# Optimization experiments

Hardware: AMD Instinct MI355X
Metric: run time of the kernel (lower is better)

## Reference

```python
import jax, jax.numpy as jnp
import numpy as np

EPS = 1e-5
NEG_INF = float('-inf')

B, L, D = 4, 1024, 1024
H = 16
HD = D // H
I = 3280  # _round_to_multiple(3.2 * 1024, 8)
WIN = 256
STD = 0.01


def rmsnorm(x, w):
    x = jnp.clip(x.astype(jnp.float32), -10000.0, 10000.0)
    rms = jnp.sqrt(jnp.maximum(jnp.mean(x * x, axis=-1, keepdims=True), EPS) + EPS)
    out = x / rms * w
    return jnp.where(jnp.isfinite(out), out, jnp.zeros_like(out))


def setup_inputs() -> dict:
    key = jax.random.key(0)
    ks = jax.random.split(key, 12)
    inp = {
        'x': jax.random.normal(ks[0], (B, L, D), dtype=jnp.float32),
        'wq_w': jax.random.normal(ks[1], (D, D), dtype=jnp.float32) * STD,
        'wq_b': jnp.zeros((D,), jnp.float32),
        'wk_w': jax.random.normal(ks[2], (D, D), dtype=jnp.float32) * STD,
        'wk_b': jnp.zeros((D,), jnp.float32),
        'wv_w': jax.random.normal(ks[3], (D, D), dtype=jnp.float32) * STD,
        'wv_b': jnp.zeros((D,), jnp.float32),
        'wo_w': jax.random.normal(ks[4], (D, D), dtype=jnp.float32) * STD,
        'wo_b': jnp.zeros((D,), jnp.float32),
        'q_norm_w': jnp.ones((HD,), jnp.float32),
        'k_norm_w': jnp.ones((HD,), jnp.float32),
        'seq_norm_w': jnp.ones((D,), jnp.float32),
        'seq_post_norm_w': jnp.ones((D,), jnp.float32),
        'ffn_norm_w': jnp.ones((D,), jnp.float32),
        'ffn_post_norm_w': jnp.ones((D,), jnp.float32),
        'w1_w': jax.random.normal(ks[5], (I, D), dtype=jnp.float32) * STD,
        'w1_b': jnp.zeros((I,), jnp.float32),
        'w2_w': jax.random.normal(ks[6], (D, I), dtype=jnp.float32) * STD,
        'w2_b': jnp.zeros((D,), jnp.float32),
        'w3_w': jax.random.normal(ks[7], (I, D), dtype=jnp.float32) * STD,
        'w3_b': jnp.zeros((I,), jnp.float32),
        'window_size': WIN,
    }
    return inp


def attention(x, wq_w, wq_b, wk_w, wk_b, wv_w, wv_b, wo_w, wo_b, q_norm_w, k_norm_w, window_size):
    b, l, d = x.shape
    x = x.astype(jnp.float32)
    q = (x @ wq_w.T + wq_b).reshape(b, l, H, HD)
    k = (x @ wk_w.T + wk_b).reshape(b, l, H, HD)
    v = (x @ wv_w.T + wv_b).reshape(b, l, H, HD)
    q = rmsnorm(q, q_norm_w)
    k = rmsnorm(k, k_norm_w)
    scale = HD ** -0.5
    scores = jnp.einsum('blhd,bmhd->bhlm', q, k) * scale
    i = jnp.arange(l)[:, None]
    j = jnp.arange(l)[None, :]
    masked = (j > i) | (i - j >= window_size)  # True => forbidden
    scores = scores + jnp.where(masked, NEG_INF, 0.0)
    p = jax.nn.softmax(scores, axis=-1)
    attn = jnp.einsum('bhlm,bmhd->blhd', p, v)
    attn = jnp.where(jnp.isfinite(attn), attn, jnp.zeros_like(attn))
    attn = attn.reshape(b, l, d)
    return attn @ wo_w.T + wo_b


def swiglu(x, w1_w, w1_b, w2_w, w2_b, w3_w, w3_b):
    x = x.astype(jnp.float32)
    z1 = x @ w1_w.T + w1_b
    z3 = x @ w3_w.T + w3_b
    return (jax.nn.silu(z1) * z3) @ w2_w.T + w2_b


def reference(x, wq_w, wq_b, wk_w, wk_b, wv_w, wv_b, wo_w, wo_b,
              q_norm_w, k_norm_w, seq_norm_w, seq_post_norm_w,
              ffn_norm_w, ffn_post_norm_w,
              w1_w, w1_b, w2_w, w2_b, w3_w, w3_b, window_size):
    # seq_norm -> attn -> seq_post_norm -> residual
    a = attention(rmsnorm(x, seq_norm_w), wq_w, wq_b, wk_w, wk_b, wv_w, wv_b,
                  wo_w, wo_b, q_norm_w, k_norm_w, window_size)
    h = x + rmsnorm(a, seq_post_norm_w)
    # ffn_norm -> ffn -> ffn_post_norm -> residual
    f = swiglu(rmsnorm(h, ffn_norm_w), w1_w, w1_b, w2_w, w2_b, w3_w, w3_b)
    return h + rmsnorm(f, ffn_post_norm_w)
```

## Files before the change

kernel.cpp:

```cpp
#include <hip/hip_runtime.h>
#include <cmath>
#include <cstdint>

typedef __bf16 bf16;
typedef bf16 bf16x4 __attribute__((ext_vector_type(4)));
typedef bf16 bf16x8 __attribute__((ext_vector_type(8)));
typedef float f32x4 __attribute__((ext_vector_type(4)));
typedef unsigned int u32;
typedef u32 u32x4 __attribute__((ext_vector_type(4)));

#define EPS 1e-5f

__device__ __forceinline__ float clipf(float v) {
    return fminf(fmaxf(v, -10000.0f), 10000.0f);
}
__device__ __forceinline__ float fin0(float v) { return isfinite(v) ? v : 0.0f; }

__device__ __forceinline__ void async_copy16(void* lds, const void* g) {
    __builtin_amdgcn_global_load_lds((__attribute__((address_space(1))) void*)(void*)g,
                                     (__attribute__((address_space(3))) void*)lds,
                                     16, 0, 0);
}

__global__ __launch_bounds__(256) void prep(const float* __restrict__ wq, const float* __restrict__ wk,
                                            const float* __restrict__ wv, const float* __restrict__ wo,
                                            bf16* __restrict__ Wq, bf16* __restrict__ Wk,
                                            bf16* __restrict__ Wv, bf16* __restrict__ Wo,
                                            const float* __restrict__ w1, const float* __restrict__ w3,
                                            bf16* __restrict__ Wf,
                                            const float* __restrict__ w2, bf16* __restrict__ W2p,
                                            const float* __restrict__ x, const float* __restrict__ snw,
                                            bf16* __restrict__ xn) {
    const int bid = blockIdx.x, t = threadIdx.x;
    if (bid < 4096) {
        int z = bid >> 10, r = bid & 1023;
        const float* in = (z == 0) ? wq : (z == 1) ? wk : (z == 2) ? wv : wo;
        bf16* out = (z == 0) ? Wq : (z == 1) ? Wk : (z == 2) ? Wv : Wo;
        f32x4 v = ((const f32x4*)(in + (size_t)r * 1024))[t];
        bf16x4 o = {(bf16)v[0], (bf16)v[1], (bf16)v[2], (bf16)v[3]};
        ((bf16x4*)(out + (size_t)r * 1024))[t] = o;
    } else if (bid < 10752) {
        int ri = bid - 4096;
        int lc = ((ri >> 5) << 4) + (ri & 15);
        const float* in = ((ri >> 4) & 1) ? w3 : w1;
        bf16x4 o = {(bf16)0.f, (bf16)0.f, (bf16)0.f, (bf16)0.f};
        if (lc < 3280) {
            f32x4 v = ((const f32x4*)(in + (size_t)lc * 1024))[t];
            o[0] = (bf16)v[0]; o[1] = (bf16)v[1]; o[2] = (bf16)v[2]; o[3] = (bf16)v[3];
        }
        ((bf16x4*)(Wf + (size_t)ri * 1024))[t] = o;
    } else if (bid < 11776) {
        int r = bid - 10752;
        for (int c4 = t * 4; c4 < 3328; c4 += 1024) {
            bf16x4 o = {(bf16)0.f, (bf16)0.f, (bf16)0.f, (bf16)0.f};
            if (c4 + 3 < 3280) {
                f32x4 v = *(const f32x4*)(w2 + (size_t)r * 3280 + c4);
                o[0] = (bf16)v[0]; o[1] = (bf16)v[1]; o[2] = (bf16)v[2]; o[3] = (bf16)v[3];
            } else {
                #pragma unroll
                for (int j = 0; j < 4; ++j)
                    if (c4 + j < 3280) o[j] = (bf16)w2[(size_t)r * 3280 + c4 + j];
            }
            *(bf16x4*)(W2p + (size_t)r * 3328 + c4) = o;
        }
    } else {
        __shared__ float sred[4];
        int row = bid - 11776;
        f32x4 xv = ((const f32x4*)(x + (size_t)row * 1024))[t];
        f32x4 cv;
        cv[0] = clipf(xv[0]); cv[1] = clipf(xv[1]); cv[2] = clipf(xv[2]); cv[3] = clipf(xv[3]);
        float ss = cv[0]*cv[0] + cv[1]*cv[1] + cv[2]*cv[2] + cv[3]*cv[3];
        #pragma unroll
        for (int off = 32; off >= 1; off >>= 1) ss += __shfl_xor(ss, off, 64);
        if ((t & 63) == 0) sred[t >> 6] = ss;
        __syncthreads();
        float tot = sred[0] + sred[1] + sred[2] + sred[3];
        float rms = sqrtf(fmaxf(tot * (1.0f / 1024.0f), EPS) + EPS);
        f32x4 wv_ = ((const f32x4*)snw)[t];
        bf16x4 o;
        o[0] = (bf16)fin0(cv[0] / rms * wv_[0]);
        o[1] = (bf16)fin0(cv[1] / rms * wv_[1]);
        o[2] = (bf16)fin0(cv[2] / rms * wv_[2]);
        o[3] = (bf16)fin0(cv[3] / rms * wv_[3]);
        *(bf16x4*)(xn + (size_t)row * 1024 + t * 4) = o;
    }
}

__global__ __launch_bounds__(256) void gemm_qkv(const bf16* __restrict__ A,
                                                const bf16* __restrict__ B0,
                                                const bf16* __restrict__ B1,
                                                const bf16* __restrict__ B2,
                                                const float* __restrict__ g0,
                                                const float* __restrict__ g1,
                                                const float* __restrict__ g2,
                                                const float* __restrict__ qnw,
                                                const float* __restrict__ knw,
                                                bf16* __restrict__ C0,
                                                bf16* __restrict__ C1,
                                                bf16* __restrict__ VT) {
    const int z = blockIdx.z;
    const bf16* B = (z == 0) ? B0 : (z == 1) ? B1 : B2;
    const float* bias = (z == 0) ? g0 : (z == 1) ? g1 : g2;
    const float* hw = (z == 0) ? qnw : knw;

    __shared__ __align__(16) bf16 sA[2][128 * 32];
    __shared__ __align__(16) bf16 sB[2][128 * 32];
    const int tid = threadIdx.x;
    const int w = tid >> 6, lane = tid & 63;
    const int m0 = blockIdx.x * 128;
    const int n0 = blockIdx.y * 128;
    const int mwo = (w >> 1) * 64, nwo = (w & 1) * 64;
    const int r16 = lane & 15, quad = lane >> 4;
    const int kreg = quad * 8;
    const int K = 1024, N = 1024;

    f32x4 zero = {0.f, 0.f, 0.f, 0.f};
    f32x4 acc[4][4];
    #pragma unroll
    for (int i = 0; i < 4; ++i)
        #pragma unroll
        for (int j = 0; j < 4; ++j) acc[i][j] = zero;

    const int c0 = tid, c1 = tid + 256;
    const int am0 = c0 >> 2, ak0 = (c0 & 3) << 3;
    const int am1 = c1 >> 2, ak1 = (c1 & 3) << 3;

    {
        async_copy16(&sA[0][c0 * 8], &A[(size_t)(m0 + am0) * K + ak0]);
        async_copy16(&sA[0][c1 * 8], &A[(size_t)(m0 + am1) * K + ak1]);
        async_copy16(&sB[0][c0 * 8], &B[(size_t)(n0 + am0) * K + ak0]);
        async_copy16(&sB[0][c1 * 8], &B[(size_t)(n0 + am1) * K + ak1]);
    }
    for (int kt = 0; kt < 32; ++kt) {
        __syncthreads();
        const int cur = kt & 1, nxt = cur ^ 1;
        if (kt + 1 < 32) {
            const int kb = (kt + 1) << 5;
            async_copy16(&sA[nxt][c0 * 8], &A[(size_t)(m0 + am0) * K + kb + ak0]);
            async_copy16(&sA[nxt][c1 * 8], &A[(size_t)(m0 + am1) * K + kb + ak1]);
            async_copy16(&sB[nxt][c0 * 8], &B[(size_t)(n0 + am0) * K + kb + ak0]);
            async_copy16(&sB[nxt][c1 * 8], &B[(size_t)(n0 + am1) * K + kb + ak1]);
        }
        bf16x8 af[4], bfr[4];
        #pragma unroll
        for (int i = 0; i < 4; ++i) {
            af[i]  = *(const bf16x8*)&sA[cur][(mwo + i * 16 + r16) * 32 + kreg];
            bfr[i] = *(const bf16x8*)&sB[cur][(nwo + i * 16 + r16) * 32 + kreg];
        }
        #pragma unroll
        for (int mi = 0; mi < 4; ++mi)
            #pragma unroll
            for (int ni = 0; ni < 4; ++ni)
                acc[mi][ni] = __builtin_amdgcn_mfma_f32_16x16x32_bf16(af[mi], bfr[ni], acc[mi][ni], 0, 0, 0);
    }

    float bv[4];
    #pragma unroll
    for (int ni = 0; ni < 4; ++ni) bv[ni] = bias[n0 + nwo + ni * 16 + r16];

    if (z < 2) {
        bf16* C = (z == 0) ? C0 : C1;
        float nwv[4];
        #pragma unroll
        for (int ni = 0; ni < 4; ++ni) nwv[ni] = hw[ni * 16 + r16];
        #pragma unroll
        for (int mi = 0; mi < 4; ++mi) {
            #pragma unroll
            for (int r = 0; r < 4; ++r) {
                float v[4], ss = 0.0f;
                #pragma unroll
                for (int ni = 0; ni < 4; ++ni) {
                    v[ni] = clipf(acc[mi][ni][r] + bv[ni]);
                    ss += v[ni] * v[ni];
                }
                ss += __shfl_xor(ss, 1, 64);
                ss += __shfl_xor(ss, 2, 64);
                ss += __shfl_xor(ss, 4, 64);
                ss += __shfl_xor(ss, 8, 64);
                float rms = sqrtf(fmaxf(ss * (1.0f / 64.0f), EPS) + EPS);
                int row = m0 + mwo + mi * 16 + quad * 4 + r;
                #pragma unroll
                for (int ni = 0; ni < 4; ++ni) {
                    int col = n0 + nwo + ni * 16 + r16;
                    C[(size_t)row * N + col] = (bf16)fin0(v[ni] / rms * nwv[ni]);
                }
            }
        }
    } else {
        const int b_ = m0 >> 10;
        const int tokbase = (m0 & 1023) + mwo;
        #pragma unroll
        for (int ni = 0; ni < 4; ++ni) {
            int col = n0 + nwo + ni * 16 + r16;
            int h_ = col >> 6, hd = col & 63;
            bf16* dst = VT + (((size_t)b_ * 16 + h_) * 64 + hd) * 1024;
            #pragma unroll
            for (int mi = 0; mi < 4; ++mi) {
                bf16x4 pack;
                #pragma unroll
                for (int r = 0; r < 4; ++r) pack[r] = (bf16)(acc[mi][ni][r] + bv[ni]);
                *(bf16x4*)&dst[tokbase + mi * 16 + quad * 4] = pack;
            }
        }
    }
}

__global__ __launch_bounds__(256) void attn_win(const bf16* __restrict__ q,
                                                const bf16* __restrict__ k,
                                                const bf16* __restrict__ vt,
                                                const int* __restrict__ winp,
                                                bf16* __restrict__ o) {
    __shared__ __align__(16) bf16 sQ[64 * 64];
    __shared__ __align__(16) bf16 sK[64 * 64];
    __shared__ __align__(16) bf16 sVt[64 * 80];
    __shared__ __align__(16) bf16 sP[64 * 64];
    const int tid = threadIdx.x, w = tid >> 6, lane = tid & 63;
    const int qt = blockIdx.x, h = blockIdx.y, b = blockIdx.z;
    const int q0 = qt * 64;
    const int win = *winp;
    const float scale = 0.125f;
    const int r16 = lane & 15, quad = lane >> 4;

    {
        int qr0 = tid >> 3, col0 = (tid & 7) * 8;
        async_copy16(&sQ[tid * 8], &q[(((size_t)b * 1024 + q0 + qr0) * 16 + h) * 64 + col0]);
        int c1 = tid + 256;
        int qr1 = c1 >> 3, col1 = (c1 & 7) * 8;
        async_copy16(&sQ[c1 * 8], &q[(((size_t)b * 1024 + q0 + qr1) * 16 + h) * 64 + col1]);
    }
    __syncthreads();
    bf16x8 aq0 = *(const bf16x8*)&sQ[(w * 16 + r16) * 64 + quad * 8];
    bf16x8 aq1 = *(const bf16x8*)&sQ[(w * 16 + r16) * 64 + 32 + quad * 8];

    float Lr[4];
    f32x4 zero = {0.f, 0.f, 0.f, 0.f};
    f32x4 accO[4];
    #pragma unroll
    for (int r = 0; r < 4; ++r) Lr[r] = 0.0f;
    #pragma unroll
    for (int nf = 0; nf < 4; ++nf) accO[nf] = zero;

    int lo = q0 - (win - 1); if (lo < 0) lo = 0;
    const int kt0 = lo >> 6;
    const bf16* vth = vt + ((size_t)b * 16 + h) * 64 * 1024;

    for (int kt = kt0; kt <= qt; ++kt) {
        __syncthreads();
        {
            int col0 = (tid & 7) * 8;
            async_copy16(&sK[tid * 8], &k[(((size_t)b * 1024 + kt * 64 + (tid >> 3)) * 16 + h) * 64 + col0]);
            int c1 = tid + 256;
            int col1 = (c1 & 7) * 8;
            async_copy16(&sK[c1 * 8], &k[(((size_t)b * 1024 + kt * 64 + (c1 >> 3)) * 16 + h) * 64 + col1]);
        }
        #pragma unroll
        for (int c = tid; c < 512; c += 256) {
            int hd = c >> 3, koff = (c & 7) * 8;
            *(u32x4*)&sVt[hd * 80 + koff] = *(const u32x4*)&vth[(size_t)hd * 1024 + kt * 64 + koff];
        }
        __syncthreads();

        f32x4 sf[4];
        #pragma unroll
        for (int nf = 0; nf < 4; ++nf) {
            bf16x8 bk0 = *(const bf16x8*)&sK[(nf * 16 + r16) * 64 + quad * 8];
            bf16x8 bk1 = *(const bf16x8*)&sK[(nf * 16 + r16) * 64 + 32 + quad * 8];
            f32x4 accS = zero;
            accS = __builtin_amdgcn_mfma_f32_16x16x32_bf16(aq0, bk0, accS, 0, 0, 0);
            accS = __builtin_amdgcn_mfma_f32_16x16x32_bf16(aq1, bk1, accS, 0, 0, 0);
            sf[nf] = accS;
        }

        #pragma unroll
        for (int r = 0; r < 4; ++r) {
            int i = q0 + w * 16 + quad * 4 + r;
            float ps = 0.0f;
            #pragma unroll
            for (int nf = 0; nf < 4; ++nf) {
                int j = kt * 64 + nf * 16 + r16;
                bool ok = (j <= i) && (i - j < win);
                float pv = ok ? __expf(sf[nf][r] * scale - 8.0f) : 0.0f;
                ps += pv;
                sP[(w * 16 + quad * 4 + r) * 64 + nf * 16 + r16] = (bf16)pv;
            }
            Lr[r] += ps;
        }
        __syncthreads();

        bf16x8 ap0 = *(const bf16x8*)&sP[(w * 16 + r16) * 64 + quad * 8];
        bf16x8 ap1 = *(const bf16x8*)&sP[(w * 16 + r16) * 64 + 32 + quad * 8];
        #pragma unroll
        for (int nf = 0; nf < 4; ++nf) {
            bf16x8 bv0 = *(const bf16x8*)&sVt[(nf * 16 + r16) * 80 + quad * 8];
            bf16x8 bv1 = *(const bf16x8*)&sVt[(nf * 16 + r16) * 80 + 32 + quad * 8];
            accO[nf] = __builtin_amdgcn_mfma_f32_16x16x32_bf16(ap0, bv0, accO[nf], 0, 0, 0);
            accO[nf] = __builtin_amdgcn_mfma_f32_16x16x32_bf16(ap1, bv1, accO[nf], 0, 0, 0);
        }
    }

    #pragma unroll
    for (int r = 0; r < 4; ++r) {
        float l = Lr[r];
        l += __shfl_xor(l, 1, 64);
        l += __shfl_xor(l, 2, 64);
        l += __shfl_xor(l, 4, 64);
        l += __shfl_xor(l, 8, 64);
        float inv = (l > 0.0f) ? 1.0f / l : 0.0f;
        int row = q0 + w * 16 + quad * 4 + r;
        #pragma unroll
        for (int nf = 0; nf < 4; ++nf) {
            float ov = fin0(accO[nf][r] * inv);
            o[(((size_t)b * 1024 + row) * 16 + h) * 64 + nf * 16 + r16] = (bf16)ov;
        }
    }
}

__global__ __launch_bounds__(512) void gemm_sk2(const bf16* __restrict__ A,
                                                const bf16* __restrict__ B,
                                                float* __restrict__ P,
                                                int K, int Kh) {
    __shared__ __align__(16) bf16 sA[2][256 * 32];
    __shared__ __align__(16) bf16 sB[2][128 * 32];
    const int tid = threadIdx.x;
    const int w = tid >> 6, lane = tid & 63;
    const int m0 = blockIdx.x * 256, n0 = blockIdx.y * 128;
    const int mwo = (w & 3) * 64, nwo = (w >> 2) * 64;
    const int r16 = lane & 15, quad = lane >> 4, kreg = quad * 8;
    const int kbase = blockIdx.z * Kh;
    const int N = 1024;

    const int ar0 = tid >> 2,        ak0 = (tid & 3) << 3;
    const int c1 = tid + 512;
    const int ar1 = c1 >> 2,         ak1 = (c1 & 3) << 3;
    const int br = tid >> 2,         bk = (tid & 3) << 3;

    f32x4 zero = {0.f, 0.f, 0.f, 0.f};
    f32x4 acc[4][4];
    #pragma unroll
    for (int i = 0; i < 4; ++i)
        #pragma unroll
        for (int j = 0; j < 4; ++j) acc[i][j] = zero;

    {
        async_copy16(&sA[0][tid * 8], &A[(size_t)(m0 + ar0) * K + kbase + ak0]);
        async_copy16(&sA[0][c1 * 8],  &A[(size_t)(m0 + ar1) * K + kbase + ak1]);
        async_copy16(&sB[0][tid * 8], &B[(size_t)(n0 + br) * K + kbase + bk]);
    }
    const int kIters = Kh >> 5;
    for (int kt = 0; kt < kIters; ++kt) {
        __syncthreads();
        const int cur = kt & 1, nxt = cur ^ 1;
        if (kt + 1 < kIters) {
            const int kb = kbase + ((kt + 1) << 5);
            async_copy16(&sA[nxt][tid * 8], &A[(size_t)(m0 + ar0) * K + kb + ak0]);
            async_copy16(&sA[nxt][c1 * 8],  &A[(size_t)(m0 + ar1) * K + kb + ak1]);
            async_copy16(&sB[nxt][tid * 8], &B[(size_t)(n0 + br) * K + kb + bk]);
        }
        bf16x8 af[4], bfr[4];
        #pragma unroll
        for (int i = 0; i < 4; ++i) {
            af[i]  = *(const bf16x8*)&sA[cur][(mwo + i * 16 + r16) * 32 + kreg];
            bfr[i] = *(const bf16x8*)&sB[cur][(nwo + i * 16 + r16) * 32 + kreg];
        }
        #pragma unroll
        for (int mi = 0; mi < 4; ++mi)
            #pragma unroll
            for (int ni = 0; ni < 4; ++ni)
                acc[mi][ni] = __builtin_amdgcn_mfma_f32_16x16x32_bf16(af[mi], bfr[ni], acc[mi][ni], 0, 0, 0);
    }

    float* Pz = P + (size_t)blockIdx.z * 4096 * 1024;
    #pragma unroll
    for (int mi = 0; mi < 4; ++mi)
        #pragma unroll
        for (int ni = 0; ni < 4; ++ni) {
            int col = n0 + nwo + ni * 16 + r16;
            #pragma unroll
            for (int r = 0; r < 4; ++r) {
                int row = m0 + mwo + mi * 16 + quad * 4 + r;
                Pz[(size_t)row * N + col] = acc[mi][ni][r];
            }
        }
}

template <bool EMIT>
__global__ __launch_bounds__(512) void resid_norm(const float* __restrict__ xres,
                                                  const float* __restrict__ p0,
                                                  const float* __restrict__ p1,
                                                  const float* __restrict__ bias,
                                                  const float* __restrict__ wpost,
                                                  const float* __restrict__ wnext,
                                                  float* __restrict__ hout,
                                                  bf16* __restrict__ hnout) {
    __shared__ float sred[8];
    const int tid = threadIdx.x;
    const int grp = tid >> 8, t = tid & 255;
    const int w4 = (tid >> 6) & 3;
    for (int it = 0; it < 4; ++it) {
        int row = it * 1024 + blockIdx.x * 2 + grp;
        f32x4 a0 = ((const f32x4*)(p0 + (size_t)row * 1024))[t];
        f32x4 a1 = ((const f32x4*)(p1 + (size_t)row * 1024))[t];
        f32x4 bv = ((const f32x4*)bias)[t];
        f32x4 af;
        af[0] = clipf(a0[0] + a1[0] + bv[0]);
        af[1] = clipf(a0[1] + a1[1] + bv[1]);
        af[2] = clipf(a0[2] + a1[2] + bv[2]);
        af[3] = clipf(a0[3] + a1[3] + bv[3]);
        float ss = af[0]*af[0] + af[1]*af[1] + af[2]*af[2] + af[3]*af[3];
        #pragma unroll
        for (int off = 32; off >= 1; off >>= 1) ss += __shfl_xor(ss, off, 64);
        __syncthreads();
        if ((tid & 63) == 0) sred[grp * 4 + w4] = ss;
        __syncthreads();
        float tot = sred[grp*4+0] + sred[grp*4+1] + sred[grp*4+2] + sred[grp*4+3];
        float rms1 = sqrtf(fmaxf(tot * (1.0f / 1024.0f), EPS) + EPS);
        f32x4 xv = ((const f32x4*)(xres + (size_t)row * 1024))[t];
        f32x4 wp = ((const f32x4*)wpost)[t];
        f32x4 hv;
        hv[0] = xv[0] + fin0(af[0] / rms1 * wp[0]);
        hv[1] = xv[1] + fin0(af[1] / rms1 * wp[1]);
        hv[2] = xv[2] + fin0(af[2] / rms1 * wp[2]);
        hv[3] = xv[3] + fin0(af[3] / rms1 * wp[3]);
        ((f32x4*)(hout + (size_t)row * 1024))[t] = hv;
        if (EMIT) {
            f32x4 cv;
            cv[0] = clipf(hv[0]); cv[1] = clipf(hv[1]); cv[2] = clipf(hv[2]); cv[3] = clipf(hv[3]);
            float ss2 = cv[0]*cv[0] + cv[1]*cv[1] + cv[2]*cv[2] + cv[3]*cv[3];
            #pragma unroll
            for (int off = 32; off >= 1; off >>= 1) ss2 += __shfl_xor(ss2, off, 64);
            __syncthreads();
            if ((tid & 63) == 0) sred[grp * 4 + w4] = ss2;
            __syncthreads();
            float tot2 = sred[grp*4+0] + sred[grp*4+1] + sred[grp*4+2] + sred[grp*4+3];
            float rms2 = sqrtf(fmaxf(tot2 * (1.0f / 1024.0f), EPS) + EPS);
            f32x4 wn = ((const f32x4*)wnext)[t];
            bf16x4 o;
            o[0] = (bf16)fin0(cv[0] / rms2 * wn[0]);
            o[1] = (bf16)fin0(cv[1] / rms2 * wn[1]);
            o[2] = (bf16)fin0(cv[2] / rms2 * wn[2]);
            o[3] = (bf16)fin0(cv[3] / rms2 * wn[3]);
            *(bf16x4*)(hnout + (size_t)row * 1024 + t * 4) = o;
        }
    }
}

template <int MB>
__device__ __forceinline__ void mphase(const bf16* Ah, const bf16x8 (&breg)[4][2],
                                       f32x4 (&acc)[8][4], int r16, int koff0, int koff1) {
    const bf16* pa0 = &Ah[(MB * 16 + r16) * 64];
    const bf16* pa1 = &Ah[((MB + 1) * 16 + r16) * 64];
    bf16x8 a00 = *(const bf16x8*)&pa0[koff0];
    bf16x8 a01 = *(const bf16x8*)&pa0[koff1];
    bf16x8 a10 = *(const bf16x8*)&pa1[koff0];
    bf16x8 a11 = *(const bf16x8*)&pa1[koff1];
    __builtin_amdgcn_s_setprio(1);
    #pragma unroll
    for (int n = 0; n < 4; ++n) {
        acc[MB][n]     = __builtin_amdgcn_mfma_f32_16x16x32_bf16(a00, breg[n][0], acc[MB][n], 0, 0, 0);
        acc[MB][n]     = __builtin_amdgcn_mfma_f32_16x16x32_bf16(a01, breg[n][1], acc[MB][n], 0, 0, 0);
        acc[MB + 1][n] = __builtin_amdgcn_mfma_f32_16x16x32_bf16(a10, breg[n][0], acc[MB + 1][n], 0, 0, 0);
        acc[MB + 1][n] = __builtin_amdgcn_mfma_f32_16x16x32_bf16(a11, breg[n][1], acc[MB + 1][n], 0, 0, 0);
    }
    __builtin_amdgcn_s_setprio(0);
}

__global__ __launch_bounds__(512, 2) void gemm_ffn1_8ph(const bf16* __restrict__ A,
                                                        const bf16* __restrict__ Wf,
                                                        const float* __restrict__ b1,
                                                        const float* __restrict__ b3,
                                                        bf16* __restrict__ G) {
    __shared__ __align__(16) bf16 sA[2][2][128 * 64];
    __shared__ __align__(16) bf16 sB[2][2][128 * 64];
    const int tid = threadIdx.x;
    const int w = tid >> 6, lane = tid & 63;
    const int wr = w >> 2, wc = w & 3;
    const int r16 = lane & 15, quad = lane >> 4;

    const int flat = blockIdx.x;
    const int swb = (flat & 7) * 52 + (flat >> 3);
    const int bm = swb & 15, bn = swb >> 4;
    const int m0 = bm * 256;
    const int n0i = bn * 256;

    const int swz = r16 & 7;
    const int koff0 = ((quad ^ swz) << 3);
    const int koff1 = (((quad + 4) ^ swz) << 3);

    const int sr0 = tid >> 3, sr1 = sr0 + 64;
    const int sk0 = (((tid & 7) ^ (sr0 & 7)) << 3);

    const bf16* aSrc0 = A + (size_t)m0 * 1024;
    const bf16* aSrc1 = A + (size_t)(m0 + 128) * 1024;
    const bf16* bSrc0 = Wf + (size_t)n0i * 1024;
    const bf16* bSrc1 = Wf + (size_t)(n0i + 128) * 1024;

#define STAGE(dst, src, ktile) do {                                                        \
        async_copy16(&(dst)[tid * 8],         (src) + (size_t)sr0 * 1024 + (ktile) * 64 + sk0); \
        async_copy16(&(dst)[(tid + 512) * 8], (src) + (size_t)sr1 * 1024 + (ktile) * 64 + sk0); \
    } while (0)

    f32x4 acc[8][4];
    #pragma unroll
    for (int i = 0; i < 8; ++i)
        #pragma unroll
        for (int j = 0; j < 4; ++j) acc[i][j] = (f32x4){0.f, 0.f, 0.f, 0.f};

    STAGE(sB[0][0], bSrc0, 0); STAGE(sB[0][1], bSrc1, 0);
    STAGE(sA[0][0], aSrc0, 0); STAGE(sA[0][1], aSrc1, 0);
    STAGE(sB[1][0], bSrc0, 1); STAGE(sB[1][1], bSrc1, 1);

    for (int t = 0; t < 16; ++t) {
        const int cur = t & 1, nxt = cur ^ 1;
        const bf16* Ah = &sA[cur][wr][0];
        const bf16* Bh = &sB[cur][wc >> 1][0];
        const int rbB = (wc & 1) << 6;
        bf16x8 breg[4][2];

        __builtin_amdgcn_s_barrier();
        if (t + 1 < 16) {
            STAGE(sA[nxt][0], aSrc0, t + 1);
            STAGE(sA[nxt][1], aSrc1, t + 1);
        }
        if (t == 15) { asm volatile("s_waitcnt vmcnt(0)" ::: "memory"); }
        else         { asm volatile("s_waitcnt vmcnt(8)" ::: "memory"); }
        #pragma unroll
        for (int n = 0; n < 4; ++n) {
            const bf16* p = &Bh[(rbB + n * 16 + r16) * 64];
            breg[n][0] = *(const bf16x8*)&p[koff0];
            breg[n][1] = *(const bf16x8*)&p[koff1];
        }
        mphase<0>(Ah, breg, acc, r16, koff0, koff1);

        __builtin_amdgcn_s_barrier();
        if (t + 2 < 16) STAGE(sB[cur][0], bSrc0, t + 2);
        mphase<2>(Ah, breg, acc, r16, koff0, koff1);

        __builtin_amdgcn_s_barrier();
        if (t + 2 < 16) STAGE(sB[cur][1], bSrc1, t + 2);
        mphase<4>(Ah, breg, acc, r16, koff0, koff1);

        mphase<6>(Ah, breg, acc, r16, koff0, koff1);
    }
#undef STAGE

    #pragma unroll
    for (int m = 0; m < 8; ++m) {
        #pragma unroll
        for (int p = 0; p < 2; ++p) {
            int col = (bn * 8 + wc * 2 + p) * 16 + r16;
            float bb1 = (col < 3280) ? b1[col] : 0.0f;
            float bb3 = (col < 3280) ? b3[col] : 0.0f;
            #pragma unroll
            for (int rr = 0; rr < 4; ++rr) {
                int row = m0 + wr * 128 + m * 16 + quad * 4 + rr;
                float z1 = acc[m][2 * p][rr] + bb1;
                float z3 = acc[m][2 * p + 1][rr] + bb3;
                float s = z1 / (1.0f + __expf(-z1));
                G[(size_t)row * 3328 + col] = (bf16)(s * z3);
            }
        }
    }
}

extern "C" void kernel_launch(void* const* d_in, const int* in_sizes, int n_in,
                              void* d_out, int out_size, void* d_ws, size_t ws_size,
                              hipStream_t stream) {
    const float* x       = (const float*)d_in[0];
    const float* wq_w    = (const float*)d_in[1];
    const float* wq_b    = (const float*)d_in[2];
    const float* wk_w    = (const float*)d_in[3];
    const float* wk_b    = (const float*)d_in[4];
    const float* wv_w    = (const float*)d_in[5];
    const float* wv_b    = (const float*)d_in[6];
    const float* wo_w    = (const float*)d_in[7];
    const float* wo_b    = (const float*)d_in[8];
    const float* q_norm_w= (const float*)d_in[9];
    const float* k_norm_w= (const float*)d_in[10];
    const float* seq_norm_w      = (const float*)d_in[11];
    const float* seq_post_norm_w = (const float*)d_in[12];
    const float* ffn_norm_w      = (const float*)d_in[13];
    const float* ffn_post_norm_w = (const float*)d_in[14];
    const float* w1_w    = (const float*)d_in[15];
    const float* w1_b    = (const float*)d_in[16];
    const float* w2_w    = (const float*)d_in[17];
    const float* w2_b    = (const float*)d_in[18];
    const float* w3_w    = (const float*)d_in[19];
    const float* w3_b    = (const float*)d_in[20];
    const int*   winp    = (const int*)d_in[21];
    float* out = (float*)d_out;

    const size_t SZ_W   = 2097152;
    const size_t SZ_WP  = 6815744;
    const size_t SZ_ACT = 8388608;
    const size_t SZ_H   = 16777216;
    const size_t SZ_P   = 33554432;

    char* p = (char*)d_ws;
    bf16* Wq  = (bf16*)p; p += SZ_W;
    bf16* Wk  = (bf16*)p; p += SZ_W;
    bf16* Wv  = (bf16*)p; p += SZ_W;
    bf16* Wo  = (bf16*)p; p += SZ_W;
    bf16* Wfp = (bf16*)p; p += 2 * SZ_WP;
    bf16* W2p = (bf16*)p; p += SZ_WP;
    float* h  = (float*)p; p += SZ_H;
    bf16* hn  = (bf16*)p; p += SZ_ACT;
    float* part = (float*)p; p += SZ_P;
    float* part1 = part + (size_t)4096 * 1024;
    char* regionA = p;
    bf16* xn    = (bf16*)(regionA);
    bf16* qb    = (bf16*)(regionA + 1 * SZ_ACT);
    bf16* kb    = (bf16*)(regionA + 2 * SZ_ACT);
    bf16* vtb   = (bf16*)(regionA + 3 * SZ_ACT);
    bf16* attnb = (bf16*)(regionA + 4 * SZ_ACT);
    bf16* g     = (bf16*)(regionA);

    prep<<<dim3(15872), dim3(256), 0, stream>>>(wq_w, wk_w, wv_w, wo_w, Wq, Wk, Wv, Wo,
                                                w1_w, w3_w, Wfp, w2_w, W2p,
                                                x, seq_norm_w, xn);

    gemm_qkv<<<dim3(32, 8, 3), dim3(256), 0, stream>>>(xn, Wq, Wk, Wv, wq_b, wk_b, wv_b,
                                                       q_norm_w, k_norm_w, qb, kb, vtb);

    attn_win<<<dim3(16, 16, 4), dim3(256), 0, stream>>>(qb, kb, vtb, winp, attnb);

    gemm_sk2<<<dim3(16, 8, 2), dim3(512), 0, stream>>>(attnb, Wo, part, 1024, 512);

    resid_norm<true><<<dim3(512), dim3(512), 0, stream>>>(x, part, part1, wo_b,
                                                          seq_post_norm_w, ffn_norm_w, h, hn);

    gemm_ffn1_8ph<<<dim3(416), dim3(512), 0, stream>>>(hn, Wfp, w1_b, w3_b, g);

    gemm_sk2<<<dim3(16, 8, 2), dim3(512), 0, stream>>>(g, W2p, part, 3328, 1664);

    resid_norm<false><<<dim3(512), dim3(512), 0, stream>>>(h, part, part1, w2_b,
                                                           ffn_post_norm_w, nullptr, out, nullptr);
}
```

Measured before the change: 391.6 us.

## Software-pipeline LDS A-fragment reads and merge B restaging into one barrier phase

Restructures the FFN1 GEMM main loop so A fragments for the next MFMA quad are read from LDS before the current quad's MFMAs run, overlapping LDS latency with matrix math. It also merges the two B-tile restage phases into a single barrier and moves the vmcnt waits to the end of each iteration, with explicit sched_barriers to fix the ordering. This removes one block-wide barrier per k-step and hides LDS read latency, at the cost of more live registers and tighter hand-tuned wait counts that must match the outstanding async copies.

```diff
diff --git a/kernel.cpp b/kernel.cpp
--- a/kernel.cpp
+++ b/kernel.cpp
@@ -445,23 +445,27 @@
 }
 
 template <int MB>
-__device__ __forceinline__ void mphase(const bf16* Ah, const bf16x8 (&breg)[4][2],
-                                       f32x4 (&acc)[8][4], int r16, int koff0, int koff1) {
-    const bf16* pa0 = &Ah[(MB * 16 + r16) * 64];
-    const bf16* pa1 = &Ah[((MB + 1) * 16 + r16) * 64];
-    bf16x8 a00 = *(const bf16x8*)&pa0[koff0];
-    bf16x8 a01 = *(const bf16x8*)&pa0[koff1];
-    bf16x8 a10 = *(const bf16x8*)&pa1[koff0];
-    bf16x8 a11 = *(const bf16x8*)&pa1[koff1];
+__device__ __forceinline__ void mquad(const bf16x8 (&a)[2][2], const bf16x8 (&breg)[4][2],
+                                      f32x4 (&acc)[8][4]) {
     __builtin_amdgcn_s_setprio(1);
     #pragma unroll
     for (int n = 0; n < 4; ++n) {
-        acc[MB][n]     = __builtin_amdgcn_mfma_f32_16x16x32_bf16(a00, breg[n][0], acc[MB][n], 0, 0, 0);
-        acc[MB][n]     = __builtin_amdgcn_mfma_f32_16x16x32_bf16(a01, breg[n][1], acc[MB][n], 0, 0, 0);
-        acc[MB + 1][n] = __builtin_amdgcn_mfma_f32_16x16x32_bf16(a10, breg[n][0], acc[MB + 1][n], 0, 0, 0);
-        acc[MB + 1][n] = __builtin_amdgcn_mfma_f32_16x16x32_bf16(a11, breg[n][1], acc[MB + 1][n], 0, 0, 0);
+        acc[MB][n]     = __builtin_amdgcn_mfma_f32_16x16x32_bf16(a[0][0], breg[n][0], acc[MB][n], 0, 0, 0);
+        acc[MB][n]     = __builtin_amdgcn_mfma_f32_16x16x32_bf16(a[0][1], breg[n][1], acc[MB][n], 0, 0, 0);
+        acc[MB + 1][n] = __builtin_amdgcn_mfma_f32_16x16x32_bf16(a[1][0], breg[n][0], acc[MB + 1][n], 0, 0, 0);
+        acc[MB + 1][n] = __builtin_amdgcn_mfma_f32_16x16x32_bf16(a[1][1], breg[n][1], acc[MB + 1][n], 0, 0, 0);
     }
     __builtin_amdgcn_s_setprio(0);
+}
+
+__device__ __forceinline__ void aread(const bf16* Ah, int MB, int r16, int koff0, int koff1,
+                                      bf16x8 (&a)[2][2]) {
+    const bf16* p0 = &Ah[(MB * 16 + r16) * 64];
+    const bf16* p1 = &Ah[((MB + 1) * 16 + r16) * 64];
+    a[0][0] = *(const bf16x8*)&p0[koff0];
+    a[0][1] = *(const bf16x8*)&p0[koff1];
+    a[1][0] = *(const bf16x8*)&p1[koff0];
+    a[1][1] = *(const bf16x8*)&p1[koff1];
 }
 
 __global__ __launch_bounds__(512, 2) void gemm_ffn1_8ph(const bf16* __restrict__ A,
@@ -505,41 +509,50 @@
         #pragma unroll
         for (int j = 0; j < 4; ++j) acc[i][j] = (f32x4){0.f, 0.f, 0.f, 0.f};
 
+    STAGE(sA[0][0], aSrc0, 0); STAGE(sA[0][1], aSrc1, 0);
     STAGE(sB[0][0], bSrc0, 0); STAGE(sB[0][1], bSrc1, 0);
-    STAGE(sA[0][0], aSrc0, 0); STAGE(sA[0][1], aSrc1, 0);
     STAGE(sB[1][0], bSrc0, 1); STAGE(sB[1][1], bSrc1, 1);
+    asm volatile("s_waitcnt vmcnt(4)" ::: "memory");
+    __builtin_amdgcn_sched_barrier(0);
 
     for (int t = 0; t < 16; ++t) {
         const int cur = t & 1, nxt = cur ^ 1;
         const bf16* Ah = &sA[cur][wr][0];
         const bf16* Bh = &sB[cur][wc >> 1][0];
         const int rbB = (wc & 1) << 6;
+
+        __builtin_amdgcn_s_barrier();
+        if (t + 1 < 16) { STAGE(sA[nxt][0], aSrc0, t + 1); STAGE(sA[nxt][1], aSrc1, t + 1); }
+
         bf16x8 breg[4][2];
-
-        __builtin_amdgcn_s_barrier();
-        if (t + 1 < 16) {
-            STAGE(sA[nxt][0], aSrc0, t + 1);
-            STAGE(sA[nxt][1], aSrc1, t + 1);
-        }
-        if (t == 15) { asm volatile("s_waitcnt vmcnt(0)" ::: "memory"); }
-        else         { asm volatile("s_waitcnt vmcnt(8)" ::: "memory"); }
         #pragma unroll
         for (int n = 0; n < 4; ++n) {
             const bf16* p = &Bh[(rbB + n * 16 + r16) * 64];
             breg[n][0] = *(const bf16x8*)&p[koff0];
             breg[n][1] = *(const bf16x8*)&p[koff1];
         }
-        mphase<0>(Ah, breg, acc, r16, koff0, koff1);
-
+        bf16x8 a0[2][2], a1[2][2];
+        aread(Ah, 0, r16, koff0, koff1, a0);
+        aread(Ah, 2, r16, koff0, koff1, a1);
+        mquad<0>(a0, breg, acc);
+
+        asm volatile("s_waitcnt lgkmcnt(0)" ::: "memory");
+        __builtin_amdgcn_sched_barrier(0);
         __builtin_amdgcn_s_barrier();
-        if (t + 2 < 16) STAGE(sB[cur][0], bSrc0, t + 2);
-        mphase<2>(Ah, breg, acc, r16, koff0, koff1);
-
-        __builtin_amdgcn_s_barrier();
-        if (t + 2 < 16) STAGE(sB[cur][1], bSrc1, t + 2);
-        mphase<4>(Ah, breg, acc, r16, koff0, koff1);
-
-        mphase<6>(Ah, breg, acc, r16, koff0, koff1);
+        if (t + 2 < 16) { STAGE(sB[cur][0], bSrc0, t + 2); STAGE(sB[cur][1], bSrc1, t + 2); }
+
+        bf16x8 a2[2][2];
+        aread(Ah, 4, r16, koff0, koff1, a2);
+        mquad<2>(a1, breg, acc);
+        bf16x8 a3[2][2];
+        aread(Ah, 6, r16, koff0, koff1, a3);
+        mquad<4>(a2, breg, acc);
+        mquad<6>(a3, breg, acc);
+
+        if (t < 14)       asm volatile("s_waitcnt lgkmcnt(0) vmcnt(4)" ::: "memory");
+        else if (t == 14) asm volatile("s_waitcnt lgkmcnt(0) vmcnt(0)" ::: "memory");
+        else              asm volatile("s_waitcnt lgkmcnt(0)" ::: "memory");
+        __builtin_amdgcn_sched_barrier(0);
     }
 #undef STAGE
 
```

Result: no change. 387.2 us (-1.1%).
